# Kernel tuning notes

Measured on AMD Instinct MI355X. Metric: run time of the kernel, lower is better.

## Reference

```python
import jax, jax.numpy as jnp
import numpy as np

T, B, H = 512, 256, 512


def setup_inputs() -> dict:
    key = jax.random.key(0)
    ks = jax.random.split(key, 8)
    s = 1.0 / np.sqrt(H)
    ins = jax.random.normal(ks[0], (T, B, H), jnp.float32)
    resets = jax.random.randint(ks[1], (T, B), 0, 2).astype(bool)
    h0 = jnp.zeros((B, H), jnp.float32)  # initialize_carry -> zeros

    def w(k):
        return (jax.random.normal(k, (H, H), jnp.float32) * s).astype(jnp.float32)

    return {
        "ins": ins, "resets": resets, "h0": h0,
        "Wir": w(ks[2]), "Wiz": w(ks[3]), "Win": w(ks[4]),
        "Whr": w(ks[5]), "Whz": w(ks[6]), "Whn": w(ks[7]),
        "bir": jnp.zeros((H,), jnp.float32),
        "biz": jnp.zeros((H,), jnp.float32),
        "bin_": jnp.zeros((H,), jnp.float32),
        "bhn": jnp.zeros((H,), jnp.float32),
    }


def reference(ins, resets, h0, Wir, Wiz, Win, Whr, Whz, Whn, bir, biz, bin_, bhn):
    # Input-to-hidden projections are time-independent: do them as one big GEMM each.
    xr = jnp.einsum('tbh,hk->tbk', ins, Wir) + bir  # [T,B,H]
    xz = jnp.einsum('tbh,hk->tbk', ins, Wiz) + biz
    xn = jnp.einsum('tbh,hk->tbk', ins, Win) + bin_

    def step(h, inp):
        xr_t, xz_t, xn_t, rst = inp
        # reset masking: reinit carry to zeros where reset flag is set
        h = jnp.where(rst[:, None], jnp.zeros_like(h), h)
        # flax GRUCell: hr/hz have no bias, hn has bias bhn
        r = jax.nn.sigmoid(xr_t + h @ Whr)
        z = jax.nn.sigmoid(xz_t + h @ Whz)
        n = jnp.tanh(xn_t + r * (h @ Whn + bhn))
        h_new = (1.0 - z) * n + z * h
        return h_new, h_new  # GRUCell returns (new_h, new_h)

    _, ys = jax.lax.scan(step, h0, (xr, xz, xn, resets))
    return ys  # [T,B,H]
```

## Files before the change

kernel.cpp:

```cpp
#include <hip/hip_runtime.h>

typedef unsigned short u16;
typedef unsigned int u32;
typedef unsigned long long u64;
typedef __attribute__((ext_vector_type(8))) short bf16x8;
typedef __attribute__((ext_vector_type(4))) float f32x4;
typedef __attribute__((ext_vector_type(4))) float fvec4;

#define Tn 512
#define Bn 256
#define Hn 512
#define SLOTS 32
#define SLABB 16384
#define NSLAB 192

__device__ __forceinline__ u16 f2bf(float x){
  u32 u = __builtin_bit_cast(u32, x);
  u32 r = u + 0x7FFFu + ((u >> 16) & 1u);
  return (u16)(r >> 16);
}
__device__ __forceinline__ float bf2f(u16 x){
  return __builtin_bit_cast(float, ((u32)x) << 16);
}
__device__ __forceinline__ float sigmoid_f(float x){ return 1.0f/(1.0f + __expf(-x)); }
__device__ __forceinline__ float tanh_f(float x){ return 2.0f/(1.0f + __expf(-2.0f*x)) - 1.0f; }

__device__ __forceinline__ void dma16(const void* g, void* l) {
  __builtin_amdgcn_global_load_lds(
      (const __attribute__((address_space(1))) unsigned int*)g,
      (__attribute__((address_space(3))) unsigned int*)l,
      16, 0, 0);
}

__device__ __forceinline__ bf16x8 ldsA(const u16* buf, int m, int kk, int lane) {
  const int row = (m << 4) + (lane & 15);
  const int ke  = (kk << 5) + ((lane >> 4) << 3);
  const int byt = (row << 10) + ((ke << 1) ^ ((row & 7) << 4));
  return *(const bf16x8*)((const char*)buf + byt);
}

#define MF4(ACC) do { \
  ACC[0][0] = __builtin_amdgcn_mfma_f32_16x16x32_bf16(a0, b0, ACC[0][0], 0, 0, 0); \
  ACC[0][1] = __builtin_amdgcn_mfma_f32_16x16x32_bf16(a1, b0, ACC[0][1], 0, 0, 0); \
  ACC[1][0] = __builtin_amdgcn_mfma_f32_16x16x32_bf16(a0, b1, ACC[1][0], 0, 0, 0); \
  ACC[1][1] = __builtin_amdgcn_mfma_f32_16x16x32_bf16(a1, b1, ACC[1][1], 0, 0, 0); \
} while (0)

__global__ __launch_bounds__(256) void prep_w(
    const float* __restrict__ Wir, const float* __restrict__ Wiz, const float* __restrict__ Win,
    const float* __restrict__ Whr, const float* __restrict__ Whz, const float* __restrict__ Whn,
    u16* __restrict__ wt)
{
  int idx = blockIdx.x * 256 + threadIdx.x;
  int within = idx & 8191;
  int slab = idx >> 13;
  int wv   = within >> 9;
  int r2   = within & 511;
  int kseg = r2 >> 7;
  int c    = (r2 >> 3) & 15;
  int j    = r2 & 7;
  int half = slab & 1;
  int gk = slab >> 1;
  int g  = gk % 6;
  int kk = gk / 6;
  int k = (kk << 5) + (kseg << 3) + j;
  int n = (half << 8) + (wv << 4) + c;
  const float* W;
  switch (g) {
    case 0: W = Wir; break; case 1: W = Wiz; break; case 2: W = Win; break;
    case 3: W = Whr; break; case 4: W = Whz; break; default: W = Whn; break;
  }
  wt[idx] = f2bf(W[k * Hn + n]);
}

__global__ __launch_bounds__(1024, 4) void gru_chains(
    const float* __restrict__ ins,
    const int*   __restrict__ resets,
    const u16*   __restrict__ wt,
    const float* __restrict__ bir, const float* __restrict__ biz,
    const float* __restrict__ bin_, const float* __restrict__ bhn,
    float* __restrict__ out)
{
  __shared__ __attribute__((aligned(16))) u16 x_lds[SLOTS * 512];
  __shared__ __attribute__((aligned(16))) u16 h_lds[SLOTS * 512];
  __shared__ __attribute__((aligned(16))) char wring[4 * SLABB];
  __shared__ u32 keys[512];
  __shared__ int slot_t[SLOTS];
  __shared__ int slot_end[SLOTS];
  __shared__ int slot_active[SLOTS];
  __shared__ int slot_fresh[SLOTS];
  __shared__ int wave_cnt[16];
  __shared__ int queue_head, n_chains, n_active;

  const int tid  = threadIdx.x;
  const int b    = blockIdx.x;
  const int wv   = tid >> 6;
  const int lane = tid & 63;

  {
    u32* starts_tmp = (u32*)wring;
    int t = tid;
    int isst = 0;
    if (t < Tn) isst = (t == 0) || (resets[t * Bn + b] != 0);
    u64 mask = __ballot(isst);
    int pos = __popcll(mask & ((1ull << lane) - 1ull));
    if (lane == 0) wave_cnt[wv] = __popcll(mask);
    __syncthreads();
    if (tid == 0) {
      int s = 0;
      for (int w = 0; w < 16; ++w) { int c = wave_cnt[w]; wave_cnt[w] = s; s += c; }
      n_chains = s;
      queue_head = SLOTS;
    }
    __syncthreads();
    if (isst) starts_tmp[wave_cnt[wv] + pos] = (u32)t;
    __syncthreads();
    const int nc = n_chains;
    if (tid < 512) {
      int i = tid;
      u32 key = 0;
      if (i < nc) {
        u32 st = starts_tmp[i];
        u32 en = (i + 1 < nc) ? starts_tmp[i + 1] : (u32)Tn;
        key = ((en - st) << 16) | st;
      }
      keys[i] = key;
    }
    for (int ks = 2; ks <= 512; ks <<= 1) {
      for (int j = ks >> 1; j > 0; j >>= 1) {
        __syncthreads();
        if (tid < 512) {
          int i = tid;
          int ix = i ^ j;
          if (ix > i) {
            u32 a = keys[i], c = keys[ix];
            bool desc = ((i & ks) == 0);
            bool sw = desc ? (a < c) : (a > c);
            if (sw) { keys[i] = c; keys[ix] = a; }
          }
        }
      }
    }
    __syncthreads();
    if (tid < SLOTS) {
      if (tid < nc) {
        u32 key = keys[tid];
        slot_t[tid]   = (int)(key & 0xFFFFu);
        slot_end[tid] = (int)((key & 0xFFFFu) + (key >> 16));
        slot_active[tid] = 1;
      } else {
        slot_active[tid] = 0; slot_t[tid] = 0; slot_end[tid] = 0;
      }
      slot_fresh[tid] = 0;
    }
    if (tid == 0) n_active = (nc < SLOTS) ? nc : SLOTS;
    for (int i = tid; i < SLOTS * 512 / 2; i += 1024) ((u32*)h_lds)[i] = 0;
    __syncthreads();
  }

  #pragma unroll
  for (int i = 0; i < 2; ++i) {
    const int g   = tid + (i << 10);
    const int row = g >> 6;
    const int k0  = (g & 63) << 3;
    const int act = slot_active[row];
    const int tc  = slot_t[row];
    fvec4 f0 = (fvec4){0.f, 0.f, 0.f, 0.f}, f1 = f0;
    if (act) {
      const fvec4* src = (const fvec4*)(ins + ((size_t)tc * Bn + b) * Hn + k0);
      f0 = __builtin_nontemporal_load(src);
      f1 = __builtin_nontemporal_load(src + 1);
    }
    uint4 pk;
    pk.x = (u32)f2bf(f0.x) | ((u32)f2bf(f0.y) << 16);
    pk.y = (u32)f2bf(f0.z) | ((u32)f2bf(f0.w) << 16);
    pk.z = (u32)f2bf(f1.x) | ((u32)f2bf(f1.y) << 16);
    pk.w = (u32)f2bf(f1.z) | ((u32)f2bf(f1.w) << 16);
    const int byt = (row << 10) + ((k0 << 1) ^ ((row & 7) << 4));
    *(uint4*)((char*)x_lds + byt) = pk;
  }
  __syncthreads();

  const int colw = (wv << 4) + (lane & 15);
  float b_r[2], b_z[2], b_n[2], b_h[2];
  #pragma unroll
  for (int half = 0; half < 2; ++half) {
    const int col = (half << 8) + colw;
    b_r[half] = bir[col]; b_z[half] = biz[col]; b_n[half] = bin_[col]; b_h[half] = bhn[col];
  }

  const u32 dm_lane_off  = (u32)((wv << 10) + (lane << 4));
  const u32 lds_wave_off = (u32)(wv << 10);
  const int brd_off      = (wv << 10) + ((lane >> 4) << 8) + ((lane & 15) << 4);

  for (;;) {
    f32x4 accR[2][2], accZ[2][2], accXN[2][2], accHN[2][2];
    #pragma unroll
    for (int hh = 0; hh < 2; ++hh)
      #pragma unroll
      for (int m = 0; m < 2; ++m) {
        accR[hh][m] = (f32x4){0.f, 0.f, 0.f, 0.f};
        accZ[hh][m] = accR[hh][m]; accXN[hh][m] = accR[hh][m]; accHN[hh][m] = accR[hh][m];
      }

    {
      const char* wsrc = (const char*)wt + dm_lane_off;
      #pragma unroll
      for (int s = 0; s < 4; ++s)
        dma16(wsrc + (size_t)s * SLABB, wring + s * SLABB + lds_wave_off);
      asm volatile("s_waitcnt vmcnt(2)" ::: "memory");
      __builtin_amdgcn_sched_barrier(0);
    }

    for (int kk = 0; kk < 16; ++kk) {
      bf16x8 ax0, ax1, ah0, ah1;
      #pragma unroll
      for (int g = 0; g < 6; ++g) {
        if (g == 0) { ax0 = ldsA(x_lds, 0, kk, lane); ax1 = ldsA(x_lds, 1, kk, lane); }
        if (g == 3) { ah0 = ldsA(h_lds, 0, kk, lane); ah1 = ldsA(h_lds, 1, kk, lane); }
        const int ph  = kk * 6 + g;
        const int rb0 = (ph & 1) << 1;
        const char* bb = wring + rb0 * SLABB + brd_off;
        bf16x8 b0 = *(const bf16x8*)bb;
        bf16x8 b1 = *(const bf16x8*)(bb + SLABB);
        bf16x8 a0 = (g < 3) ? ax0 : ah0;
        bf16x8 a1 = (g < 3) ? ax1 : ah1;
        if (g == 0 || g == 3)      MF4(accR);
        else if (g == 1 || g == 4) MF4(accZ);
        else if (g == 2)           MF4(accXN);
        else                       MF4(accHN);
        asm volatile("s_waitcnt lgkmcnt(0)" ::: "memory");
        __builtin_amdgcn_sched_barrier(0);
        const int s0 = (ph << 1) + 4;
        if (s0 < NSLAB) {
          const char* wsrc = (const char*)wt + (size_t)s0 * SLABB + dm_lane_off;
          dma16(wsrc,         wring + rb0 * SLABB + lds_wave_off);
          dma16(wsrc + SLABB, wring + (rb0 + 1) * SLABB + lds_wave_off);
          asm volatile("s_waitcnt vmcnt(2)" ::: "memory");
        } else {
          asm volatile("s_waitcnt vmcnt(0)" ::: "memory");
        }
        __builtin_amdgcn_sched_barrier(0);
      }
    }

    __syncthreads();

    #pragma unroll
    for (int half = 0; half < 2; ++half) {
      const int col = (half << 8) + colw;
      const float bi_r = b_r[half], bi_z = b_z[half], bi_n = b_n[half], bh_n = b_h[half];
      #pragma unroll
      for (int m = 0; m < 2; ++m) {
        #pragma unroll
        for (int i = 0; i < 4; ++i) {
          const int slot = (m << 4) + ((lane >> 4) << 2) + i;
          float rr = sigmoid_f(accR[half][m][i] + bi_r);
          float zz = sigmoid_f(accZ[half][m][i] + bi_z);
          const int hbyt = (slot << 10) + ((col << 1) ^ ((slot & 7) << 4));
          float hold = bf2f(*(const u16*)((const char*)h_lds + hbyt));
          float nn = tanh_f(accXN[half][m][i] + bi_n + rr * (accHN[half][m][i] + bh_n));
          float hnew = (1.0f - zz) * nn + zz * hold;
          *(u16*)((char*)h_lds + hbyt) = f2bf(hnew);
          if (slot_active[slot]) {
            __builtin_nontemporal_store(hnew, out + ((size_t)slot_t[slot] * Bn + b) * Hn + col);
          }
        }
      }
    }
    __syncthreads();

    if (tid < SLOTS) {
      const int s = tid;
      int fresh = 0;
      if (slot_active[s]) {
        int nt = slot_t[s] + 1;
        if (nt >= slot_end[s]) {
          int idx = atomicAdd(&queue_head, 1);
          if (idx < n_chains) {
            u32 key = keys[idx];
            slot_t[s]   = (int)(key & 0xFFFFu);
            slot_end[s] = (int)((key & 0xFFFFu) + (key >> 16));
            fresh = 1;
          } else {
            slot_active[s] = 0;
            atomicSub(&n_active, 1);
            fresh = 1;
          }
        } else {
          slot_t[s] = nt;
        }
      }
      slot_fresh[s] = fresh;
    }
    __syncthreads();

    #pragma unroll
    for (int i = 0; i < 2; ++i) {
      const int g   = tid + (i << 10);
      const int row = g >> 6;
      const int k0  = (g & 63) << 3;
      const int act = slot_active[row];
      const int tc  = slot_t[row];
      const int kill = slot_fresh[row] | (act == 0);
      const int sbyt = (row << 10) + ((k0 << 1) ^ ((row & 7) << 4));
      if (kill) *(uint4*)((char*)h_lds + sbyt) = (uint4){0, 0, 0, 0};
      fvec4 f0 = (fvec4){0.f, 0.f, 0.f, 0.f}, f1 = f0;
      if (act) {
        const fvec4* src = (const fvec4*)(ins + ((size_t)tc * Bn + b) * Hn + k0);
        f0 = __builtin_nontemporal_load(src);
        f1 = __builtin_nontemporal_load(src + 1);
      }
      uint4 pk;
      pk.x = (u32)f2bf(f0.x) | ((u32)f2bf(f0.y) << 16);
      pk.y = (u32)f2bf(f0.z) | ((u32)f2bf(f0.w) << 16);
      pk.z = (u32)f2bf(f1.x) | ((u32)f2bf(f1.y) << 16);
      pk.w = (u32)f2bf(f1.z) | ((u32)f2bf(f1.w) << 16);
      *(uint4*)((char*)x_lds + sbyt) = pk;
    }
    __syncthreads();

    if (n_active <= 0) break;
  }
}

extern "C" void kernel_launch(void* const* d_in, const int* in_sizes, int n_in,
                              void* d_out, int out_size, void* d_ws, size_t ws_size,
                              hipStream_t stream) {
  (void)in_sizes; (void)n_in; (void)out_size; (void)ws_size;
  const float* ins    = (const float*)d_in[0];
  const int*   resets = (const int*)  d_in[1];
  const float* Wir = (const float*)d_in[3];
  const float* Wiz = (const float*)d_in[4];
  const float* Win = (const float*)d_in[5];
  const float* Whr = (const float*)d_in[6];
  const float* Whz = (const float*)d_in[7];
  const float* Whn = (const float*)d_in[8];
  const float* bir = (const float*)d_in[9];
  const float* biz = (const float*)d_in[10];
  const float* bin_ = (const float*)d_in[11];
  const float* bhn = (const float*)d_in[12];

  u16* wt = (u16*)d_ws;

  prep_w<<<6144, 256, 0, stream>>>(Wir, Wiz, Win, Whr, Whz, Whn, wt);
  gru_chains<<<Bn, 1024, 0, stream>>>(ins, resets, wt, bir, biz, bin_, bhn, (float*)d_out);
}
```

Baseline: 792.1 us.

## Deepen weight slab ring to five single-slab stages with finer-grained prefetch

Changes the LDS weight ring from four buffers consumed in pairs to five buffers consumed one slab at a time, issuing one DMA per slab and waiting with vmcnt(4). Each slab is now refilled right after it is consumed, keeping four loads in flight instead of roughly two, so global-to-LDS latency is hidden better. The kk loop is fully unrolled so buffer indices and wait counts become compile-time constants. This costs an extra 16KB of LDS, which may lower occupancy, and full unrolling grows code size and register pressure.

Measured after the change: 2.672 ms. 3.37x slower.

```diff
diff --git a/kernel.cpp b/kernel.cpp
--- a/kernel.cpp
+++ b/kernel.cpp
@@ -13,6 +13,7 @@
 #define SLOTS 32
 #define SLABB 16384
 #define NSLAB 192
+#define RING 5
 
 __device__ __forceinline__ u16 f2bf(float x){
   u32 u = __builtin_bit_cast(u32, x);
@@ -32,19 +33,20 @@
       16, 0, 0);
 }
 
+__device__ __forceinline__ void waitvm_c(int n) {
+  if (n == 4)      asm volatile("s_waitcnt vmcnt(4)" ::: "memory");
+  else if (n == 3) asm volatile("s_waitcnt vmcnt(3)" ::: "memory");
+  else if (n == 2) asm volatile("s_waitcnt vmcnt(2)" ::: "memory");
+  else if (n == 1) asm volatile("s_waitcnt vmcnt(1)" ::: "memory");
+  else if (n == 0) asm volatile("s_waitcnt vmcnt(0)" ::: "memory");
+}
+
 __device__ __forceinline__ bf16x8 ldsA(const u16* buf, int m, int kk, int lane) {
   const int row = (m << 4) + (lane & 15);
   const int ke  = (kk << 5) + ((lane >> 4) << 3);
   const int byt = (row << 10) + ((ke << 1) ^ ((row & 7) << 4));
   return *(const bf16x8*)((const char*)buf + byt);
 }
-
-#define MF4(ACC) do { \
-  ACC[0][0] = __builtin_amdgcn_mfma_f32_16x16x32_bf16(a0, b0, ACC[0][0], 0, 0, 0); \
-  ACC[0][1] = __builtin_amdgcn_mfma_f32_16x16x32_bf16(a1, b0, ACC[0][1], 0, 0, 0); \
-  ACC[1][0] = __builtin_amdgcn_mfma_f32_16x16x32_bf16(a0, b1, ACC[1][0], 0, 0, 0); \
-  ACC[1][1] = __builtin_amdgcn_mfma_f32_16x16x32_bf16(a1, b1, ACC[1][1], 0, 0, 0); \
-} while (0)
 
 __global__ __launch_bounds__(256) void prep_w(
     const float* __restrict__ Wir, const float* __restrict__ Wiz, const float* __restrict__ Win,
@@ -83,7 +85,7 @@
 {
   __shared__ __attribute__((aligned(16))) u16 x_lds[SLOTS * 512];
   __shared__ __attribute__((aligned(16))) u16 h_lds[SLOTS * 512];
-  __shared__ __attribute__((aligned(16))) char wring[4 * SLABB];
+  __shared__ __attribute__((aligned(16))) char wring[RING * SLABB];
   __shared__ u32 keys[512];
   __shared__ int slot_t[SLOTS];
   __shared__ int slot_end[SLOTS];
@@ -206,41 +208,50 @@
     {
       const char* wsrc = (const char*)wt + dm_lane_off;
       #pragma unroll
-      for (int s = 0; s < 4; ++s)
+      for (int s = 0; s < RING; ++s)
         dma16(wsrc + (size_t)s * SLABB, wring + s * SLABB + lds_wave_off);
-      asm volatile("s_waitcnt vmcnt(2)" ::: "memory");
+      waitvm_c(4);
       __builtin_amdgcn_sched_barrier(0);
     }
 
+    #pragma unroll
     for (int kk = 0; kk < 16; ++kk) {
       bf16x8 ax0, ax1, ah0, ah1;
       #pragma unroll
       for (int g = 0; g < 6; ++g) {
         if (g == 0) { ax0 = ldsA(x_lds, 0, kk, lane); ax1 = ldsA(x_lds, 1, kk, lane); }
         if (g == 3) { ah0 = ldsA(h_lds, 0, kk, lane); ah1 = ldsA(h_lds, 1, kk, lane); }
-        const int ph  = kk * 6 + g;
-        const int rb0 = (ph & 1) << 1;
-        const char* bb = wring + rb0 * SLABB + brd_off;
-        bf16x8 b0 = *(const bf16x8*)bb;
-        bf16x8 b1 = *(const bf16x8*)(bb + SLABB);
         bf16x8 a0 = (g < 3) ? ax0 : ah0;
         bf16x8 a1 = (g < 3) ? ax1 : ah1;
-        if (g == 0 || g == 3)      MF4(accR);
-        else if (g == 1 || g == 4) MF4(accZ);
-        else if (g == 2)           MF4(accXN);
-        else                       MF4(accHN);
-        asm volatile("s_waitcnt lgkmcnt(0)" ::: "memory");
-        __builtin_amdgcn_sched_barrier(0);
-        const int s0 = (ph << 1) + 4;
-        if (s0 < NSLAB) {
-          const char* wsrc = (const char*)wt + (size_t)s0 * SLABB + dm_lane_off;
-          dma16(wsrc,         wring + rb0 * SLABB + lds_wave_off);
-          dma16(wsrc + SLABB, wring + (rb0 + 1) * SLABB + lds_wave_off);
-          asm volatile("s_waitcnt vmcnt(2)" ::: "memory");
-        } else {
-          asm volatile("s_waitcnt vmcnt(0)" ::: "memory");
+        #pragma unroll
+        for (int half = 0; half < 2; ++half) {
+          const int p   = (kk * 6 + g) * 2 + half;
+          const int buf = p % RING;
+          bf16x8 bb = *(const bf16x8*)(wring + buf * SLABB + brd_off);
+          if (g == 0 || g == 3) {
+            accR[half][0] = __builtin_amdgcn_mfma_f32_16x16x32_bf16(a0, bb, accR[half][0], 0, 0, 0);
+            accR[half][1] = __builtin_amdgcn_mfma_f32_16x16x32_bf16(a1, bb, accR[half][1], 0, 0, 0);
+          } else if (g == 1 || g == 4) {
+            accZ[half][0] = __builtin_amdgcn_mfma_f32_16x16x32_bf16(a0, bb, accZ[half][0], 0, 0, 0);
+            accZ[half][1] = __builtin_amdgcn_mfma_f32_16x16x32_bf16(a1, bb, accZ[half][1], 0, 0, 0);
+          } else if (g == 2) {
+            accXN[half][0] = __builtin_amdgcn_mfma_f32_16x16x32_bf16(a0, bb, accXN[half][0], 0, 0, 0);
+            accXN[half][1] = __builtin_amdgcn_mfma_f32_16x16x32_bf16(a1, bb, accXN[half][1], 0, 0, 0);
+          } else {
+            accHN[half][0] = __builtin_amdgcn_mfma_f32_16x16x32_bf16(a0, bb, accHN[half][0], 0, 0, 0);
+            accHN[half][1] = __builtin_amdgcn_mfma_f32_16x16x32_bf16(a1, bb, accHN[half][1], 0, 0, 0);
+          }
+          asm volatile("s_waitcnt lgkmcnt(0)" ::: "memory");
+          __builtin_amdgcn_sched_barrier(0);
+          if (p + RING < NSLAB) {
+            const char* wsrc = (const char*)wt + (size_t)(p + RING) * SLABB + dm_lane_off;
+            dma16(wsrc, wring + buf * SLABB + lds_wave_off);
+            waitvm_c(4);
+          } else if (p < NSLAB - 1) {
+            waitvm_c(NSLAB - 2 - p);
+          }
+          __builtin_amdgcn_sched_barrier(0);
         }
-        __builtin_amdgcn_sched_barrier(0);
       }
     }
 
```

## Double-buffer slot state, prefetch weight ring early, and drop per-step barriers

Applied to the files above, without the earlier changes.

Slot scheduling state moves into double-buffered arrays, and the next step's slot update is computed at the start of each step so it overlaps the MFMA loop. This removes two __syncthreads per recurrent step, and the h reset now happens inside the gate epilogue. The initial weight-ring DMA for the next step is issued right after the MFMA loop and before the epilogue, so its latency hides behind the gate math. The per-phase lgkmcnt(0) wait and one sched_barrier are also removed, which risks LDS read/DMA-overwrite races in the ring buffer.

After: 797.1 us. No clear change (+0.6%).

```diff
diff --git a/kernel.cpp b/kernel.cpp
--- a/kernel.cpp
+++ b/kernel.cpp
@@ -85,12 +85,13 @@
   __shared__ __attribute__((aligned(16))) u16 h_lds[SLOTS * 512];
   __shared__ __attribute__((aligned(16))) char wring[4 * SLABB];
   __shared__ u32 keys[512];
-  __shared__ int slot_t[SLOTS];
-  __shared__ int slot_end[SLOTS];
-  __shared__ int slot_active[SLOTS];
-  __shared__ int slot_fresh[SLOTS];
+  __shared__ int slot_t[2][SLOTS];
+  __shared__ int slot_end[2][SLOTS];
+  __shared__ int slot_active[2][SLOTS];
+  __shared__ int slot_fresh[2][SLOTS];
+  __shared__ int n_act[2];
   __shared__ int wave_cnt[16];
-  __shared__ int queue_head, n_chains, n_active;
+  __shared__ int queue_head, n_chains;
 
   const int tid  = threadIdx.x;
   const int b    = blockIdx.x;
@@ -145,26 +146,38 @@
     if (tid < SLOTS) {
       if (tid < nc) {
         u32 key = keys[tid];
-        slot_t[tid]   = (int)(key & 0xFFFFu);
-        slot_end[tid] = (int)((key & 0xFFFFu) + (key >> 16));
-        slot_active[tid] = 1;
+        slot_t[0][tid]   = (int)(key & 0xFFFFu);
+        slot_end[0][tid] = (int)((key & 0xFFFFu) + (key >> 16));
+        slot_active[0][tid] = 1;
       } else {
-        slot_active[tid] = 0; slot_t[tid] = 0; slot_end[tid] = 0;
-      }
-      slot_fresh[tid] = 0;
-    }
-    if (tid == 0) n_active = (nc < SLOTS) ? nc : SLOTS;
+        slot_active[0][tid] = 0; slot_t[0][tid] = 0; slot_end[0][tid] = 0;
+      }
+      slot_fresh[0][tid] = 0;
+    }
+    if (tid == 0) n_act[0] = (nc < SLOTS) ? nc : SLOTS;
     for (int i = tid; i < SLOTS * 512 / 2; i += 1024) ((u32*)h_lds)[i] = 0;
     __syncthreads();
   }
+
+  const int colw = (wv << 4) + (lane & 15);
+  float b_r[2], b_z[2], b_n[2], b_h[2];
+  #pragma unroll
+  for (int half = 0; half < 2; ++half) {
+    const int col = (half << 8) + colw;
+    b_r[half] = bir[col]; b_z[half] = biz[col]; b_n[half] = bin_[col]; b_h[half] = bhn[col];
+  }
+
+  const u32 dm_lane_off  = (u32)((wv << 10) + (lane << 4));
+  const u32 lds_wave_off = (u32)(wv << 10);
+  const int brd_off      = (wv << 10) + ((lane >> 4) << 8) + ((lane & 15) << 4);
 
   #pragma unroll
   for (int i = 0; i < 2; ++i) {
     const int g   = tid + (i << 10);
     const int row = g >> 6;
     const int k0  = (g & 63) << 3;
-    const int act = slot_active[row];
-    const int tc  = slot_t[row];
+    const int act = slot_active[0][row];
+    const int tc  = slot_t[0][row];
     fvec4 f0 = (fvec4){0.f, 0.f, 0.f, 0.f}, f1 = f0;
     if (act) {
       const fvec4* src = (const fvec4*)(ins + ((size_t)tc * Bn + b) * Hn + k0);
@@ -179,21 +192,46 @@
     const int byt = (row << 10) + ((k0 << 1) ^ ((row & 7) << 4));
     *(uint4*)((char*)x_lds + byt) = pk;
   }
+  {
+    const char* wsrc = (const char*)wt + dm_lane_off;
+    #pragma unroll
+    for (int s = 0; s < 4; ++s)
+      dma16(wsrc + (size_t)s * SLABB, wring + s * SLABB + lds_wave_off);
+    __builtin_amdgcn_sched_barrier(0);
+  }
   __syncthreads();
 
-  const int colw = (wv << 4) + (lane & 15);
-  float b_r[2], b_z[2], b_n[2], b_h[2];
-  #pragma unroll
-  for (int half = 0; half < 2; ++half) {
-    const int col = (half << 8) + colw;
-    b_r[half] = bir[col]; b_z[half] = biz[col]; b_n[half] = bin_[col]; b_h[half] = bhn[col];
-  }
-
-  const u32 dm_lane_off  = (u32)((wv << 10) + (lane << 4));
-  const u32 lds_wave_off = (u32)(wv << 10);
-  const int brd_off      = (wv << 10) + ((lane >> 4) << 8) + ((lane & 15) << 4);
+  int cp = 0;
 
   for (;;) {
+    const int np = cp ^ 1;
+
+    if (tid < SLOTS) {
+      const int s = tid;
+      int act = slot_active[cp][s];
+      int t   = slot_t[cp][s];
+      int en  = slot_end[cp][s];
+      int fresh = 0;
+      if (act) {
+        int nt2 = t + 1;
+        if (nt2 >= en) {
+          int idx = atomicAdd(&queue_head, 1);
+          if (idx < n_chains) {
+            u32 key = keys[idx];
+            t = (int)(key & 0xFFFFu); en = t + (int)(key >> 16); fresh = 1;
+          } else {
+            act = 0; fresh = 1;
+          }
+        } else {
+          t = nt2;
+        }
+      }
+      slot_t[np][s] = t; slot_end[np][s] = en;
+      slot_active[np][s] = act; slot_fresh[np][s] = fresh;
+      u64 am = __ballot(act != 0);
+      if (tid == 0) n_act[np] = __popcll(am);
+    }
+
     f32x4 accR[2][2], accZ[2][2], accXN[2][2], accHN[2][2];
     #pragma unroll
     for (int hh = 0; hh < 2; ++hh)
@@ -202,15 +240,6 @@
         accR[hh][m] = (f32x4){0.f, 0.f, 0.f, 0.f};
         accZ[hh][m] = accR[hh][m]; accXN[hh][m] = accR[hh][m]; accHN[hh][m] = accR[hh][m];
       }
-
-    {
-      const char* wsrc = (const char*)wt + dm_lane_off;
-      #pragma unroll
-      for (int s = 0; s < 4; ++s)
-        dma16(wsrc + (size_t)s * SLABB, wring + s * SLABB + lds_wave_off);
-      asm volatile("s_waitcnt vmcnt(2)" ::: "memory");
-      __builtin_amdgcn_sched_barrier(0);
-    }
 
     for (int kk = 0; kk < 16; ++kk) {
       bf16x8 ax0, ax1, ah0, ah1;
@@ -220,16 +249,15 @@
         if (g == 3) { ah0 = ldsA(h_lds, 0, kk, lane); ah1 = ldsA(h_lds, 1, kk, lane); }
         const int ph  = kk * 6 + g;
         const int rb0 = (ph & 1) << 1;
-        const char* bb = wring + rb0 * SLABB + brd_off;
-        bf16x8 b0 = *(const bf16x8*)bb;
-        bf16x8 b1 = *(const bf16x8*)(bb + SLABB);
+        const char* bbp = wring + rb0 * SLABB + brd_off;
+        bf16x8 b0 = *(const bf16x8*)bbp;
+        bf16x8 b1 = *(const bf16x8*)(bbp + SLABB);
         bf16x8 a0 = (g < 3) ? ax0 : ah0;
         bf16x8 a1 = (g < 3) ? ax1 : ah1;
         if (g == 0 || g == 3)      MF4(accR);
         else if (g == 1 || g == 4) MF4(accZ);
         else if (g == 2)           MF4(accXN);
         else                       MF4(accHN);
-        asm volatile("s_waitcnt lgkmcnt(0)" ::: "memory");
         __builtin_amdgcn_sched_barrier(0);
         const int s0 = (ph << 1) + 4;
         if (s0 < NSLAB) {
@@ -240,11 +268,18 @@
         } else {
           asm volatile("s_waitcnt vmcnt(0)" ::: "memory");
         }
-        __builtin_amdgcn_sched_barrier(0);
-      }
-    }
-
-    __syncthreads();
+      }
+    }
+
+    __syncthreads();
+
+    {
+      const char* wsrc = (const char*)wt + dm_lane_off;
+      #pragma unroll
+      for (int s = 0; s < 4; ++s)
+        dma16(wsrc + (size_t)s * SLABB, wring + s * SLABB + lds_wave_off);
+      __builtin_amdgcn_sched_barrier(0);
+    }
 
     #pragma unroll
     for (int half = 0; half < 2; ++half) {
@@ -261,50 +296,23 @@
           float hold = bf2f(*(const u16*)((const char*)h_lds + hbyt));
           float nn = tanh_f(accXN[half][m][i] + bi_n + rr * (accHN[half][m][i] + bh_n));
           float hnew = (1.0f - zz) * nn + zz * hold;
-          *(u16*)((char*)h_lds + hbyt) = f2bf(hnew);
-          if (slot_active[slot]) {
-            __builtin_nontemporal_store(hnew, out + ((size_t)slot_t[slot] * Bn + b) * Hn + col);
+          const int kill = slot_fresh[np][slot] | (slot_active[np][slot] == 0);
+          *(u16*)((char*)h_lds + hbyt) = f2bf(kill ? 0.0f : hnew);
+          if (slot_active[cp][slot]) {
+            __builtin_nontemporal_store(hnew,
+                out + ((size_t)slot_t[cp][slot] * Bn + b) * Hn + col);
           }
         }
       }
     }
-    __syncthreads();
-
-    if (tid < SLOTS) {
-      const int s = tid;
-      int fresh = 0;
-      if (slot_active[s]) {
-        int nt = slot_t[s] + 1;
-        if (nt >= slot_end[s]) {
-          int idx = atomicAdd(&queue_head, 1);
-          if (idx < n_chains) {
-            u32 key = keys[idx];
-            slot_t[s]   = (int)(key & 0xFFFFu);
-            slot_end[s] = (int)((key & 0xFFFFu) + (key >> 16));
-            fresh = 1;
-          } else {
-            slot_active[s] = 0;
-            atomicSub(&n_active, 1);
-            fresh = 1;
-          }
-        } else {
-          slot_t[s] = nt;
-        }
-      }
-      slot_fresh[s] = fresh;
-    }
-    __syncthreads();
 
     #pragma unroll
     for (int i = 0; i < 2; ++i) {
       const int g   = tid + (i << 10);
       const int row = g >> 6;
       const int k0  = (g & 63) << 3;
-      const int act = slot_active[row];
-      const int tc  = slot_t[row];
-      const int kill = slot_fresh[row] | (act == 0);
-      const int sbyt = (row << 10) + ((k0 << 1) ^ ((row & 7) << 4));
-      if (kill) *(uint4*)((char*)h_lds + sbyt) = (uint4){0, 0, 0, 0};
+      const int act = slot_active[np][row];
+      const int tc  = slot_t[np][row];
       fvec4 f0 = (fvec4){0.f, 0.f, 0.f, 0.f}, f1 = f0;
       if (act) {
         const fvec4* src = (const fvec4*)(ins + ((size_t)tc * Bn + b) * Hn + k0);
@@ -316,11 +324,14 @@
       pk.y = (u32)f2bf(f0.z) | ((u32)f2bf(f0.w) << 16);
       pk.z = (u32)f2bf(f1.x) | ((u32)f2bf(f1.y) << 16);
       pk.w = (u32)f2bf(f1.z) | ((u32)f2bf(f1.w) << 16);
-      *(uint4*)((char*)x_lds + sbyt) = pk;
-    }
-    __syncthreads();
-
-    if (n_active <= 0) break;
+      const int byt = (row << 10) + ((k0 << 1) ^ ((row & 7) << 4));
+      *(uint4*)((char*)x_lds + byt) = pk;
+    }
+
+    __syncthreads();
+
+    if (n_act[np] <= 0) break;
+    cp = np;
   }
 }
 
```
